# Performance work log

Hardware: AMD Instinct MI355X
Metric: run time of the kernel (lower is better)

The kernel has to match this reference:

```python
import jax, jax.numpy as jnp
import numpy as np

N_NODES = 50000
N_EDGES = 800000


def _gcn_conv(x, W, b, src, dst, n_nodes):
    # GCNConv(normalize=False): out[i] = sum_{(j->i) in E} (x_j @ W) + b
    h = x @ W                                   # [N, d_out]
    agg = jax.ops.segment_sum(h[src], dst, num_segments=n_nodes)  # [N, d_out]
    return agg + b


def setup_inputs() -> dict:
    key = jax.random.key(0)
    ks = jax.random.split(key, 10)
    nfeat, nhid, nclass = 500, 64, 50
    inp = {
        "features": jax.random.normal(ks[0], (N_NODES, nfeat), dtype=jnp.float32),
        "edge_index": jax.random.randint(ks[1], (2, N_EDGES), 0, N_NODES, dtype=jnp.int64),
        "W1": jax.random.normal(ks[2], (nfeat, nhid), dtype=jnp.float32) * (1.0 / np.sqrt(nfeat)),
        "b1": jax.random.normal(ks[3], (nhid,), dtype=jnp.float32) * 0.01,
        "Wc1": jax.random.normal(ks[4], (nhid, nhid), dtype=jnp.float32) * (1.0 / np.sqrt(nhid)),
        "bc1": jax.random.normal(ks[5], (nhid,), dtype=jnp.float32) * 0.01,
        "Wc2": jax.random.normal(ks[6], (2 * nhid, 2 * nhid), dtype=jnp.float32) * (1.0 / np.sqrt(2 * nhid)),
        "bc2": jax.random.normal(ks[7], (2 * nhid,), dtype=jnp.float32) * 0.01,
        "W2": jax.random.normal(ks[8], (7 * nhid, nclass), dtype=jnp.float32) * (1.0 / np.sqrt(7 * nhid)),
        "b2": jax.random.normal(ks[9], (nclass,), dtype=jnp.float32) * 0.01,
    }
    return inp


def reference(features, edge_index, W1, b1, Wc1, bc1, Wc2, bc2, W2, b2):
    n = features.shape[0]
    src, dst = edge_index[0], edge_index[1]  # PyG: messages flow row(src) -> col(dst)

    x = jax.nn.relu(features @ W1 + b1)                       # [N, nhid]
    x11 = _gcn_conv(x, Wc1, bc1, src, dst, n)                 # [N, nhid]
    x12 = _gcn_conv(x11, Wc1, bc1, src, dst, n)               # [N, nhid]
    x1 = jnp.concatenate((x11, x12), axis=-1)                 # [N, 2*nhid]
    x21 = _gcn_conv(x1, Wc2, bc2, src, dst, n)                # [N, 2*nhid]
    x22 = _gcn_conv(x21, Wc2, bc2, src, dst, n)               # [N, 2*nhid]
    x2 = jnp.concatenate((x21, x22), axis=-1)                 # [N, 4*nhid]
    h = jnp.concatenate((x, x1, x2), axis=-1)                 # [N, 7*nhid]
    # dropout omitted (deterministic inference reference)
    return jax.nn.sigmoid(h @ W2 + b2)                        # [N, nclass]
```

## Files before the change

### kernel.cpp

```cpp
#include <hip/hip_runtime.h>
#include <math.h>

#define N_NODES 50000
#define N_EDGES 800000

typedef short bf16x8 __attribute__((ext_vector_type(8)));
typedef float f32x4 __attribute__((ext_vector_type(4)));

__device__ __forceinline__ ushort f2bf(float f) {
    unsigned u = __float_as_uint(f);
    u += 0x7fffu + ((u >> 16) & 1u);
    return (ushort)(u >> 16);
}
__device__ __forceinline__ float bf2f(ushort h) {
    return __uint_as_float(((unsigned)h) << 16);
}
__device__ __forceinline__ void split2(float a, ushort& h, ushort& l) {
    h = f2bf(a);
    l = f2bf(a - bf2f(h));
}

__global__ __launch_bounds__(256) void convert_wt_kernel(
    const float* __restrict__ W, int K, int N, int KP, int NP,
    ushort* __restrict__ Th, ushort* __restrict__ Tl)
{
    int i = blockIdx.x * 256 + threadIdx.x;
    if (i >= NP * KP) return;
    int n = i / KP, k = i % KP;
    float v = (k < K && n < N) ? W[(size_t)k * N + n] : 0.f;
    ushort h, l;
    split2(v, h, l);
    Th[(size_t)n * KP + k] = h;
    Tl[(size_t)n * KP + k] = l;
}

__device__ __forceinline__ void stage_B_lds(
    const ushort* __restrict__ WTh, const ushort* __restrict__ WTl,
    int n0, int KP, int k0, ushort* sBh, ushort* sBl, int tid)
{
    for (int i = tid; i < 512; i += 256) {
        int pl = i >> 8, s = i & 255, row = s >> 2, q = s & 3;
        const ushort* src = pl ? WTl : WTh;
        uint4 v = *(const uint4*)&src[(size_t)(n0 + row) * KP + k0 + q * 8];
        ushort* d = pl ? sBl : sBh;
        *(uint4*)&d[row * 40 + q * 8] = v;
    }
}

__device__ __forceinline__ void stage_A_planes(
    const ushort* __restrict__ Ahi, const ushort* __restrict__ Alo,
    int lda, int brow, int M, int k0, ushort* sAh, ushort* sAl, int tid)
{
    for (int i = tid; i < 1024; i += 256) {
        int pl = i >> 9, s = i & 511, row = s >> 2, q = s & 3;
        int gr = brow + row;
        uint4 v = make_uint4(0u, 0u, 0u, 0u);
        const ushort* src = pl ? Alo : Ahi;
        if (gr < M) v = *(const uint4*)&src[(size_t)gr * lda + k0 + q * 8];
        ushort* d = pl ? sAl : sAh;
        *(uint4*)&d[row * 40 + q * 8] = v;
    }
}

__device__ __forceinline__ void mfma_compute(
    const ushort* sAh, const ushort* sAl,
    const ushort* sBh, const ushort* sBl,
    int lane, int wr, int wc, f32x4 acc[4][2])
{
    bf16x8 ah[4], al[4], bh[2], bl[2];
#pragma unroll
    for (int mi = 0; mi < 4; ++mi) {
        int off = (wr + mi * 16 + (lane & 15)) * 40 + (lane >> 4) * 8;
        ah[mi] = *(const bf16x8*)&sAh[off];
        al[mi] = *(const bf16x8*)&sAl[off];
    }
#pragma unroll
    for (int ni = 0; ni < 2; ++ni) {
        int off = (wc + ni * 16 + (lane & 15)) * 40 + (lane >> 4) * 8;
        bh[ni] = *(const bf16x8*)&sBh[off];
        bl[ni] = *(const bf16x8*)&sBl[off];
    }
#pragma unroll
    for (int mi = 0; mi < 4; ++mi)
#pragma unroll
        for (int ni = 0; ni < 2; ++ni) {
            acc[mi][ni] = __builtin_amdgcn_mfma_f32_16x16x32_bf16(ah[mi], bh[ni], acc[mi][ni], 0, 0, 0);
            acc[mi][ni] = __builtin_amdgcn_mfma_f32_16x16x32_bf16(ah[mi], bl[ni], acc[mi][ni], 0, 0, 0);
            acc[mi][ni] = __builtin_amdgcn_mfma_f32_16x16x32_bf16(al[mi], bh[ni], acc[mi][ni], 0, 0, 0);
        }
}

template<int K, int ACT>
__global__ __launch_bounds__(256) void gemm_mfma_kernel(
    const ushort* __restrict__ Ahi, const ushort* __restrict__ Alo, int lda,
    const ushort* __restrict__ WTh, const ushort* __restrict__ WTl,
    const float* __restrict__ bias,
    ushort* __restrict__ Ohi, ushort* __restrict__ Olo, int ldo, int M)
{
    __shared__ ushort sAh[128 * 40], sAl[128 * 40], sBh[64 * 40], sBl[64 * 40];
    const int tid  = threadIdx.x;
    const int brow = blockIdx.x * 128;
    const int n0   = blockIdx.y * 64;
    const int lane = tid & 63, w = tid >> 6;
    const int wr = (w >> 1) * 64, wc = (w & 1) * 32;

    f32x4 acc[4][2];
#pragma unroll
    for (int mi = 0; mi < 4; ++mi)
#pragma unroll
        for (int ni = 0; ni < 2; ++ni) acc[mi][ni] = (f32x4)0.f;

    for (int ch = 0; ch < K / 32; ++ch) {
        const int k0 = ch * 32;
        stage_A_planes(Ahi, Alo, lda, brow, M, k0, sAh, sAl, tid);
        stage_B_lds(WTh, WTl, n0, K, k0, sBh, sBl, tid);
        __syncthreads();
        mfma_compute(sAh, sAl, sBh, sBl, lane, wr, wc, acc);
        __syncthreads();
    }

#pragma unroll
    for (int mi = 0; mi < 4; ++mi)
#pragma unroll
        for (int ni = 0; ni < 2; ++ni) {
            int col = n0 + wc + ni * 16 + (lane & 15);
            float b = bias[col];
#pragma unroll
            for (int r = 0; r < 4; ++r) {
                int row = brow + wr + mi * 16 + (lane >> 4) * 4 + r;
                if (row < M) {
                    float v = acc[mi][ni][r] + b;
                    if (ACT == 1) v = fmaxf(v, 0.f);
                    ushort h, l;
                    split2(v, h, l);
                    Ohi[(size_t)row * ldo + col] = h;
                    Olo[(size_t)row * ldo + col] = l;
                }
            }
        }
}

__global__ __launch_bounds__(256) void gemm_feat_kernel(
    const float* __restrict__ A,
    const ushort* __restrict__ WTh, const ushort* __restrict__ WTl,
    const float* __restrict__ bias,
    ushort* __restrict__ Ohi, ushort* __restrict__ Olo, int M)
{
    __shared__ ushort sAh[128 * 40], sAl[128 * 40], sBh[64 * 40], sBl[64 * 40];
    const int tid  = threadIdx.x;
    const int brow = blockIdx.x * 128;
    const int lane = tid & 63, w = tid >> 6;
    const int wr = (w >> 1) * 64, wc = (w & 1) * 32;

    f32x4 acc[4][2];
#pragma unroll
    for (int mi = 0; mi < 4; ++mi)
#pragma unroll
        for (int ni = 0; ni < 2; ++ni) acc[mi][ni] = (f32x4)0.f;

    for (int ch = 0; ch < 16; ++ch) {
        const int k0 = ch * 32;
        for (int i = tid; i < 1024; i += 256) {
            int row = i >> 3, q = i & 7;
            int gr = brow + row, gk = k0 + q * 4;
            float4 v = make_float4(0.f, 0.f, 0.f, 0.f);
            if (gr < M) {
                const float* ap = A + (size_t)gr * 500;
                if (gk + 3 < 500) {
                    v = *(const float4*)&ap[gk];
                } else {
                    if (gk + 0 < 500) v.x = ap[gk + 0];
                    if (gk + 1 < 500) v.y = ap[gk + 1];
                    if (gk + 2 < 500) v.z = ap[gk + 2];
                    if (gk + 3 < 500) v.w = ap[gk + 3];
                }
            }
            ushort h0, h1, h2, h3, l0, l1, l2, l3;
            split2(v.x, h0, l0); split2(v.y, h1, l1);
            split2(v.z, h2, l2); split2(v.w, h3, l3);
            uint2 hv, lv;
            hv.x = (unsigned)h0 | ((unsigned)h1 << 16);
            hv.y = (unsigned)h2 | ((unsigned)h3 << 16);
            lv.x = (unsigned)l0 | ((unsigned)l1 << 16);
            lv.y = (unsigned)l2 | ((unsigned)l3 << 16);
            *(uint2*)&sAh[row * 40 + q * 4] = hv;
            *(uint2*)&sAl[row * 40 + q * 4] = lv;
        }
        stage_B_lds(WTh, WTl, 0, 512, k0, sBh, sBl, tid);
        __syncthreads();
        mfma_compute(sAh, sAl, sBh, sBl, lane, wr, wc, acc);
        __syncthreads();
    }

#pragma unroll
    for (int mi = 0; mi < 4; ++mi)
#pragma unroll
        for (int ni = 0; ni < 2; ++ni) {
            int col = wc + ni * 16 + (lane & 15);
            float b = bias[col];
#pragma unroll
            for (int r = 0; r < 4; ++r) {
                int row = brow + wr + mi * 16 + (lane >> 4) * 4 + r;
                if (row < M) {
                    float v = fmaxf(acc[mi][ni][r] + b, 0.f);
                    ushort h, l;
                    split2(v, h, l);
                    Ohi[(size_t)row * 64 + col] = h;
                    Olo[(size_t)row * 64 + col] = l;
                }
            }
        }
}

__global__ __launch_bounds__(256) void final_mfma_kernel(
    const ushort* __restrict__ Xhi,  const ushort* __restrict__ Xlo,
    const ushort* __restrict__ X1hi, const ushort* __restrict__ X1lo,
    const ushort* __restrict__ X2hi, const ushort* __restrict__ X2lo,
    const ushort* __restrict__ WTh,  const ushort* __restrict__ WTl,
    const float* __restrict__ b2,
    float* __restrict__ out, int M)
{
    __shared__ ushort sAh[128 * 40], sAl[128 * 40], sBh[64 * 40], sBl[64 * 40];
    const int tid  = threadIdx.x;
    const int brow = blockIdx.x * 128;
    const int lane = tid & 63, w = tid >> 6;
    const int wr = (w >> 1) * 64, wc = (w & 1) * 32;

    f32x4 acc[4][2];
#pragma unroll
    for (int mi = 0; mi < 4; ++mi)
#pragma unroll
        for (int ni = 0; ni < 2; ++ni) acc[mi][ni] = (f32x4)0.f;

    for (int ch = 0; ch < 14; ++ch) {
        const ushort *Ah, *Al;
        int lda, off;
        if (ch < 2)      { Ah = Xhi;  Al = Xlo;  lda = 64;  off = ch * 32; }
        else if (ch < 6) { Ah = X1hi; Al = X1lo; lda = 128; off = (ch - 2) * 32; }
        else             { Ah = X2hi; Al = X2lo; lda = 256; off = (ch - 6) * 32; }
        stage_A_planes(Ah + off, Al + off, lda, brow, M, 0, sAh, sAl, tid);
        stage_B_lds(WTh, WTl, 0, 448, ch * 32, sBh, sBl, tid);
        __syncthreads();
        mfma_compute(sAh, sAl, sBh, sBl, lane, wr, wc, acc);
        __syncthreads();
    }

#pragma unroll
    for (int mi = 0; mi < 4; ++mi)
#pragma unroll
        for (int ni = 0; ni < 2; ++ni) {
            int col = wc + ni * 16 + (lane & 15);
            if (col < 50) {
                float b = b2[col];
#pragma unroll
                for (int r = 0; r < 4; ++r) {
                    int row = brow + wr + mi * 16 + (lane >> 4) * 4 + r;
                    if (row < M) {
                        float v = acc[mi][ni][r] + b;
                        out[(size_t)row * 50 + col] = 1.f / (1.f + expf(-v));
                    }
                }
            }
        }
}

__global__ __launch_bounds__(256) void zero_kernel(int* __restrict__ p, int n)
{
    int i = blockIdx.x * 256 + threadIdx.x;
    if (i < n) p[i] = 0;
}

__global__ __launch_bounds__(256) void count_kernel(
    const int* __restrict__ dst, int* __restrict__ counts, int ne)
{
    int e = blockIdx.x * 256 + threadIdx.x;
    if (e < ne) atomicAdd(&counts[dst[e]], 1);
}

__global__ __launch_bounds__(256) void scan1_kernel(
    const int* __restrict__ counts, int* __restrict__ local,
    int* __restrict__ bsum, int n)
{
    __shared__ int sd[256];
    const int t = threadIdx.x;
    const int i = blockIdx.x * 256 + t;
    int c = (i < n) ? counts[i] : 0;
    sd[t] = c;
    __syncthreads();
#pragma unroll
    for (int off = 1; off < 256; off <<= 1) {
        int v = (t >= off) ? sd[t - off] : 0;
        __syncthreads();
        sd[t] += v;
        __syncthreads();
    }
    if (i < n) local[i] = sd[t] - c;
    if (t == 255) bsum[blockIdx.x] = sd[255];
}

__global__ __launch_bounds__(256) void scan2_kernel(
    const int* __restrict__ bsum, int* __restrict__ boff, int nb)
{
    __shared__ int sd[256];
    const int t = threadIdx.x;
    int v = (t < nb) ? bsum[t] : 0;
    sd[t] = v;
    __syncthreads();
#pragma unroll
    for (int off = 1; off < 256; off <<= 1) {
        int u = (t >= off) ? sd[t - off] : 0;
        __syncthreads();
        sd[t] += u;
        __syncthreads();
    }
    if (t < nb) boff[t] = sd[t] - v;
}

__global__ __launch_bounds__(256) void scan3_kernel(
    int* __restrict__ row_ptr, const int* __restrict__ boff,
    int* __restrict__ cursor, int n, int total)
{
    const int i = blockIdx.x * 256 + threadIdx.x;
    if (i < n) {
        int v = row_ptr[i] + boff[blockIdx.x];
        row_ptr[i] = v;
        cursor[i]  = v;
    }
    if (i == 0) row_ptr[n] = total;
}

__global__ __launch_bounds__(256) void fill_kernel(
    const int* __restrict__ src, const int* __restrict__ dst,
    int* __restrict__ cursor, int* __restrict__ elist, int ne)
{
    int e = blockIdx.x * 256 + threadIdx.x;
    if (e < ne) {
        int p = atomicAdd(&cursor[dst[e]], 1);
        elist[p] = src[e];
    }
}

template<int D>
__global__ __launch_bounds__(256) void agg_planes_kernel(
    const ushort* __restrict__ hhi, const ushort* __restrict__ hlo, int ldh,
    const int* __restrict__ row_ptr, const int* __restrict__ elist,
    ushort* __restrict__ ohi, ushort* __restrict__ olo, int ldo, int n)
{
    constexpr int LPR = D / 4;
    constexpr int EPI = 64 / LPR;
    const int lane = threadIdx.x & 63;
    const int node = blockIdx.x * 4 + (threadIdx.x >> 6);
    if (node >= n) return;
    const int g  = lane / LPR;
    const int c4 = (lane % LPR) * 4;
    const int beg = row_ptr[node], end = row_ptr[node + 1];

    float a0 = 0.f, a1 = 0.f, a2 = 0.f, a3 = 0.f;
    for (int e = beg + g; e < end; e += EPI) {
        int s = elist[e];
        uint2 hv = *(const uint2*)&hhi[(size_t)s * ldh + c4];
        uint2 lv = *(const uint2*)&hlo[(size_t)s * ldh + c4];
        a0 += bf2f((ushort)hv.x) + bf2f((ushort)lv.x);
        a1 += bf2f((ushort)(hv.x >> 16)) + bf2f((ushort)(lv.x >> 16));
        a2 += bf2f((ushort)hv.y) + bf2f((ushort)lv.y);
        a3 += bf2f((ushort)(hv.y >> 16)) + bf2f((ushort)(lv.y >> 16));
    }
    if (EPI == 4) {
        a0 += __shfl_xor(a0, 16); a1 += __shfl_xor(a1, 16);
        a2 += __shfl_xor(a2, 16); a3 += __shfl_xor(a3, 16);
    }
    a0 += __shfl_xor(a0, 32); a1 += __shfl_xor(a1, 32);
    a2 += __shfl_xor(a2, 32); a3 += __shfl_xor(a3, 32);

    if (g == 0) {
        ushort h0, h1, h2, h3, l0, l1, l2, l3;
        split2(a0, h0, l0); split2(a1, h1, l1);
        split2(a2, h2, l2); split2(a3, h3, l3);
        uint2 hv, lv;
        hv.x = (unsigned)h0 | ((unsigned)h1 << 16);
        hv.y = (unsigned)h2 | ((unsigned)h3 << 16);
        lv.x = (unsigned)l0 | ((unsigned)l1 << 16);
        lv.y = (unsigned)l2 | ((unsigned)l3 << 16);
        *(uint2*)&ohi[(size_t)node * ldo + c4] = hv;
        *(uint2*)&olo[(size_t)node * ldo + c4] = lv;
    }
}

extern "C" void kernel_launch(void* const* d_in, const int* in_sizes, int n_in,
                              void* d_out, int out_size, void* d_ws, size_t ws_size,
                              hipStream_t stream)
{
    const float* features = (const float*)d_in[0];
    const int*   ei       = (const int*)d_in[1];
    const float* W1  = (const float*)d_in[2];
    const float* b1  = (const float*)d_in[3];
    const float* Wc1 = (const float*)d_in[4];
    const float* bc1 = (const float*)d_in[5];
    const float* Wc2 = (const float*)d_in[6];
    const float* bc2 = (const float*)d_in[7];
    const float* W2  = (const float*)d_in[8];
    const float* b2  = (const float*)d_in[9];
    float* out = (float*)d_out;

    const int* src = ei;
    const int* dst = ei + N_EDGES;

    ushort* Xhi  = (ushort*)d_ws;
    ushort* Xlo  = Xhi  + (size_t)N_NODES * 64;
    ushort* X1hi = Xlo  + (size_t)N_NODES * 64;
    ushort* X1lo = X1hi + (size_t)N_NODES * 128;
    ushort* X2hi = X1lo + (size_t)N_NODES * 128;
    ushort* X2lo = X2hi + (size_t)N_NODES * 256;
    ushort* Ghi  = X2lo + (size_t)N_NODES * 256;
    ushort* Glo  = Ghi  + (size_t)N_NODES * 128;
    ushort* W1Th  = Glo  + (size_t)N_NODES * 128;
    ushort* W1Tl  = W1Th  + 64 * 512;
    ushort* Wc1Th = W1Tl  + 64 * 512;
    ushort* Wc1Tl = Wc1Th + 64 * 64;
    ushort* Wc2Th = Wc1Tl + 64 * 64;
    ushort* Wc2Tl = Wc2Th + 128 * 128;
    ushort* W2Th  = Wc2Tl + 128 * 128;
    ushort* W2Tl  = W2Th  + 64 * 448;
    int* counts  = (int*)(W2Tl + 64 * 448);
    int* cursor  = counts + N_NODES;
    int* row_ptr = cursor + N_NODES;
    int* elist   = row_ptr + (N_NODES + 1);
    int* bsum    = elist + N_EDGES;
    int* boff    = bsum + 256;

    const int MB = (N_NODES + 127) / 128;
    const int EB = (N_EDGES + 255) / 256;
    const int NB = (N_NODES + 255) / 256;
    const int AB = (N_NODES + 3) / 4;

    zero_kernel<<<NB, 256, 0, stream>>>(counts, N_NODES);
    count_kernel<<<EB, 256, 0, stream>>>(dst, counts, N_EDGES);
    scan1_kernel<<<NB, 256, 0, stream>>>(counts, row_ptr, bsum, N_NODES);
    scan2_kernel<<<1, 256, 0, stream>>>(bsum, boff, NB);
    scan3_kernel<<<NB, 256, 0, stream>>>(row_ptr, boff, cursor, N_NODES, N_EDGES);
    fill_kernel<<<EB, 256, 0, stream>>>(src, dst, cursor, elist, N_EDGES);

    convert_wt_kernel<<<(64 * 512 + 255) / 256, 256, 0, stream>>>(W1, 500, 64, 512, 64, W1Th, W1Tl);
    convert_wt_kernel<<<(64 * 64 + 255) / 256, 256, 0, stream>>>(Wc1, 64, 64, 64, 64, Wc1Th, Wc1Tl);
    convert_wt_kernel<<<(128 * 128 + 255) / 256, 256, 0, stream>>>(Wc2, 128, 128, 128, 128, Wc2Th, Wc2Tl);
    convert_wt_kernel<<<(64 * 448 + 255) / 256, 256, 0, stream>>>(W2, 448, 50, 448, 64, W2Th, W2Tl);

    gemm_feat_kernel<<<MB, 256, 0, stream>>>(features, W1Th, W1Tl, b1, Xhi, Xlo, N_NODES);

    agg_planes_kernel<64><<<AB, 256, 0, stream>>>(Xhi, Xlo, 64, row_ptr, elist, Ghi, Glo, 128, N_NODES);
    gemm_mfma_kernel<64, 0><<<dim3(MB, 1), 256, 0, stream>>>(
        Ghi, Glo, 128, Wc1Th, Wc1Tl, bc1, X1hi, X1lo, 128, N_NODES);

    agg_planes_kernel<64><<<AB, 256, 0, stream>>>(X1hi, X1lo, 128, row_ptr, elist, Ghi, Glo, 128, N_NODES);
    gemm_mfma_kernel<64, 0><<<dim3(MB, 1), 256, 0, stream>>>(
        Ghi, Glo, 128, Wc1Th, Wc1Tl, bc1, X1hi + 64, X1lo + 64, 128, N_NODES);

    agg_planes_kernel<64><<<AB, 256, 0, stream>>>(X1hi + 64, X1lo + 64, 128, row_ptr, elist,
                                                  Ghi + 64, Glo + 64, 128, N_NODES);
    gemm_mfma_kernel<128, 0><<<dim3(MB, 2), 256, 0, stream>>>(
        Ghi, Glo, 128, Wc2Th, Wc2Tl, bc2, X2hi, X2lo, 256, N_NODES);

    agg_planes_kernel<128><<<AB, 256, 0, stream>>>(X2hi, X2lo, 256, row_ptr, elist, Ghi, Glo, 128, N_NODES);
    gemm_mfma_kernel<128, 0><<<dim3(MB, 2), 256, 0, stream>>>(
        Ghi, Glo, 128, Wc2Th, Wc2Tl, bc2, X2hi + 128, X2lo + 128, 256, N_NODES);

    final_mfma_kernel<<<MB, 256, 0, stream>>>(Xhi, Xlo, X1hi, X1lo, X2hi, X2lo,
                                              W2Th, W2Tl, b2, out, N_NODES);
}
```

Baseline: 576.0 us.

## Register-prefetch GEMM tiles, shrink row tile to 64, unroll edge aggregation by two

The GEMM kernels now prefetch the next K-chunk of A and B into registers while the MFMAs run on the current LDS tile. This hides global load latency behind compute. The row tile also drops from 128 to 64, which doubles the block count for better occupancy and SM fill but reuses B less per block. The aggregation loop is unrolled by two so more gather loads are in flight per lane.

```diff
diff --git a/kernel.cpp b/kernel.cpp
--- a/kernel.cpp
+++ b/kernel.cpp
@@ -34,42 +34,56 @@
     Tl[(size_t)n * KP + k] = l;
 }
 
-__device__ __forceinline__ void stage_B_lds(
+__device__ __forceinline__ void loadA_planes(
+    const ushort* __restrict__ Ahi, const ushort* __restrict__ Alo,
+    int lda, int brow, int M, int k0, int tid, uint4* pA)
+{
+#pragma unroll
+    for (int j = 0; j < 2; ++j) {
+        int i = j * 256 + tid;
+        int pl = i >> 8, s = i & 255, row = s >> 2, q = s & 3;
+        int gr = brow + row;
+        const ushort* src = pl ? Alo : Ahi;
+        uint4 v = make_uint4(0u, 0u, 0u, 0u);
+        if (gr < M) v = *(const uint4*)&src[(size_t)gr * lda + k0 + q * 8];
+        pA[j] = v;
+    }
+}
+
+__device__ __forceinline__ void loadB_planes(
     const ushort* __restrict__ WTh, const ushort* __restrict__ WTl,
-    int n0, int KP, int k0, ushort* sBh, ushort* sBl, int tid)
-{
-    for (int i = tid; i < 512; i += 256) {
+    int n0, int KP, int k0, int tid, uint4* pB)
+{
+#pragma unroll
+    for (int j = 0; j < 2; ++j) {
+        int i = j * 256 + tid;
         int pl = i >> 8, s = i & 255, row = s >> 2, q = s & 3;
         const ushort* src = pl ? WTl : WTh;
-        uint4 v = *(const uint4*)&src[(size_t)(n0 + row) * KP + k0 + q * 8];
-        ushort* d = pl ? sBl : sBh;
-        *(uint4*)&d[row * 40 + q * 8] = v;
-    }
-}
-
-__device__ __forceinline__ void stage_A_planes(
-    const ushort* __restrict__ Ahi, const ushort* __restrict__ Alo,
-    int lda, int brow, int M, int k0, ushort* sAh, ushort* sAl, int tid)
-{
-    for (int i = tid; i < 1024; i += 256) {
-        int pl = i >> 9, s = i & 511, row = s >> 2, q = s & 3;
-        int gr = brow + row;
-        uint4 v = make_uint4(0u, 0u, 0u, 0u);
-        const ushort* src = pl ? Alo : Ahi;
-        if (gr < M) v = *(const uint4*)&src[(size_t)gr * lda + k0 + q * 8];
-        ushort* d = pl ? sAl : sAh;
-        *(uint4*)&d[row * 40 + q * 8] = v;
-    }
-}
-
-__device__ __forceinline__ void mfma_compute(
+        pB[j] = *(const uint4*)&src[(size_t)(n0 + row) * KP + k0 + q * 8];
+    }
+}
+
+__device__ __forceinline__ void writeAB(
+    ushort* sAh, ushort* sAl, ushort* sBh, ushort* sBl,
+    int tid, const uint4* pA, const uint4* pB)
+{
+#pragma unroll
+    for (int j = 0; j < 2; ++j) {
+        int i = j * 256 + tid;
+        int pl = i >> 8, s = i & 255, row = s >> 2, q = s & 3;
+        *(uint4*)&(pl ? sAl : sAh)[row * 40 + q * 8] = pA[j];
+        *(uint4*)&(pl ? sBl : sBh)[row * 40 + q * 8] = pB[j];
+    }
+}
+
+__device__ __forceinline__ void mfma_2x2(
     const ushort* sAh, const ushort* sAl,
     const ushort* sBh, const ushort* sBl,
-    int lane, int wr, int wc, f32x4 acc[4][2])
-{
-    bf16x8 ah[4], al[4], bh[2], bl[2];
-#pragma unroll
-    for (int mi = 0; mi < 4; ++mi) {
+    int lane, int wr, int wc, f32x4 acc[2][2])
+{
+    bf16x8 ah[2], al[2], bh[2], bl[2];
+#pragma unroll
+    for (int mi = 0; mi < 2; ++mi) {
         int off = (wr + mi * 16 + (lane & 15)) * 40 + (lane >> 4) * 8;
         ah[mi] = *(const bf16x8*)&sAh[off];
         al[mi] = *(const bf16x8*)&sAl[off];
@@ -81,7 +95,7 @@
         bl[ni] = *(const bf16x8*)&sBl[off];
     }
 #pragma unroll
-    for (int mi = 0; mi < 4; ++mi)
+    for (int mi = 0; mi < 2; ++mi)
 #pragma unroll
         for (int ni = 0; ni < 2; ++ni) {
             acc[mi][ni] = __builtin_amdgcn_mfma_f32_16x16x32_bf16(ah[mi], bh[ni], acc[mi][ni], 0, 0, 0);
@@ -97,30 +111,37 @@
     const float* __restrict__ bias,
     ushort* __restrict__ Ohi, ushort* __restrict__ Olo, int ldo, int M)
 {
-    __shared__ ushort sAh[128 * 40], sAl[128 * 40], sBh[64 * 40], sBl[64 * 40];
+    constexpr int NCH = K / 32;
+    __shared__ ushort sAh[64 * 40], sAl[64 * 40], sBh[64 * 40], sBl[64 * 40];
     const int tid  = threadIdx.x;
-    const int brow = blockIdx.x * 128;
+    const int brow = blockIdx.x * 64;
     const int n0   = blockIdx.y * 64;
     const int lane = tid & 63, w = tid >> 6;
-    const int wr = (w >> 1) * 64, wc = (w & 1) * 32;
-
-    f32x4 acc[4][2];
-#pragma unroll
-    for (int mi = 0; mi < 4; ++mi)
+    const int wr = (w >> 1) * 32, wc = (w & 1) * 32;
+
+    f32x4 acc[2][2];
+#pragma unroll
+    for (int mi = 0; mi < 2; ++mi)
 #pragma unroll
         for (int ni = 0; ni < 2; ++ni) acc[mi][ni] = (f32x4)0.f;
 
-    for (int ch = 0; ch < K / 32; ++ch) {
-        const int k0 = ch * 32;
-        stage_A_planes(Ahi, Alo, lda, brow, M, k0, sAh, sAl, tid);
-        stage_B_lds(WTh, WTl, n0, K, k0, sBh, sBl, tid);
-        __syncthreads();
-        mfma_compute(sAh, sAl, sBh, sBl, lane, wr, wc, acc);
-        __syncthreads();
-    }
-
-#pragma unroll
-    for (int mi = 0; mi < 4; ++mi)
+    uint4 pA[2], pB[2];
+    loadA_planes(Ahi, Alo, lda, brow, M, 0, tid, pA);
+    loadB_planes(WTh, WTl, n0, K, 0, tid, pB);
+
+    for (int ch = 0; ch < NCH; ++ch) {
+        writeAB(sAh, sAl, sBh, sBl, tid, pA, pB);
+        __syncthreads();
+        if (ch + 1 < NCH) {
+            loadA_planes(Ahi, Alo, lda, brow, M, (ch + 1) * 32, tid, pA);
+            loadB_planes(WTh, WTl, n0, K, (ch + 1) * 32, tid, pB);
+        }
+        mfma_2x2(sAh, sAl, sBh, sBl, lane, wr, wc, acc);
+        __syncthreads();
+    }
+
+#pragma unroll
+    for (int mi = 0; mi < 2; ++mi)
 #pragma unroll
         for (int ni = 0; ni < 2; ++ni) {
             int col = n0 + wc + ni * 16 + (lane & 15);
@@ -146,22 +167,26 @@
     const float* __restrict__ bias,
     ushort* __restrict__ Ohi, ushort* __restrict__ Olo, int M)
 {
-    __shared__ ushort sAh[128 * 40], sAl[128 * 40], sBh[64 * 40], sBl[64 * 40];
+    __shared__ ushort sAh[64 * 40], sAl[64 * 40], sBh[64 * 40], sBl[64 * 40];
     const int tid  = threadIdx.x;
-    const int brow = blockIdx.x * 128;
+    const int brow = blockIdx.x * 64;
     const int lane = tid & 63, w = tid >> 6;
-    const int wr = (w >> 1) * 64, wc = (w & 1) * 32;
-
-    f32x4 acc[4][2];
-#pragma unroll
-    for (int mi = 0; mi < 4; ++mi)
+    const int wr = (w >> 1) * 32, wc = (w & 1) * 32;
+
+    f32x4 acc[2][2];
+#pragma unroll
+    for (int mi = 0; mi < 2; ++mi)
 #pragma unroll
         for (int ni = 0; ni < 2; ++ni) acc[mi][ni] = (f32x4)0.f;
 
-    for (int ch = 0; ch < 16; ++ch) {
-        const int k0 = ch * 32;
-        for (int i = tid; i < 1024; i += 256) {
-            int row = i >> 3, q = i & 7;
+    const int frow = tid >> 2, fq = (tid & 3);
+    float4 pA[2];
+    uint4  pB[2];
+
+    auto loadA_feat = [&](int k0) {
+#pragma unroll
+        for (int j = 0; j < 2; ++j) {
+            int row = frow, q = fq + j * 4;
             int gr = brow + row, gk = k0 + q * 4;
             float4 v = make_float4(0.f, 0.f, 0.f, 0.f);
             if (gr < M) {
@@ -175,9 +200,16 @@
                     if (gk + 3 < 500) v.w = ap[gk + 3];
                 }
             }
+            pA[j] = v;
+        }
+    };
+    auto writeA_feat = [&]() {
+#pragma unroll
+        for (int j = 0; j < 2; ++j) {
+            int row = frow, q = fq + j * 4;
             ushort h0, h1, h2, h3, l0, l1, l2, l3;
-            split2(v.x, h0, l0); split2(v.y, h1, l1);
-            split2(v.z, h2, l2); split2(v.w, h3, l3);
+            split2(pA[j].x, h0, l0); split2(pA[j].y, h1, l1);
+            split2(pA[j].z, h2, l2); split2(pA[j].w, h3, l3);
             uint2 hv, lv;
             hv.x = (unsigned)h0 | ((unsigned)h1 << 16);
             hv.y = (unsigned)h2 | ((unsigned)h3 << 16);
@@ -186,14 +218,30 @@
             *(uint2*)&sAh[row * 40 + q * 4] = hv;
             *(uint2*)&sAl[row * 40 + q * 4] = lv;
         }
-        stage_B_lds(WTh, WTl, 0, 512, k0, sBh, sBl, tid);
-        __syncthreads();
-        mfma_compute(sAh, sAl, sBh, sBl, lane, wr, wc, acc);
-        __syncthreads();
-    }
-
-#pragma unroll
-    for (int mi = 0; mi < 4; ++mi)
+    };
+
+    loadA_feat(0);
+    loadB_planes(WTh, WTl, 0, 512, 0, tid, pB);
+
+    for (int ch = 0; ch < 16; ++ch) {
+        writeA_feat();
+#pragma unroll
+        for (int j = 0; j < 2; ++j) {
+            int i = j * 256 + tid;
+            int pl = i >> 8, s = i & 255, row = s >> 2, q = s & 3;
+            *(uint4*)&(pl ? sBl : sBh)[row * 40 + q * 8] = pB[j];
+        }
+        __syncthreads();
+        if (ch + 1 < 16) {
+            loadA_feat((ch + 1) * 32);
+            loadB_planes(WTh, WTl, 0, 512, (ch + 1) * 32, tid, pB);
+        }
+        mfma_2x2(sAh, sAl, sBh, sBl, lane, wr, wc, acc);
+        __syncthreads();
+    }
+
+#pragma unroll
+    for (int mi = 0; mi < 2; ++mi)
 #pragma unroll
         for (int ni = 0; ni < 2; ++ni) {
             int col = wc + ni * 16 + (lane & 15);
@@ -220,33 +268,47 @@
     const float* __restrict__ b2,
     float* __restrict__ out, int M)
 {
-    __shared__ ushort sAh[128 * 40], sAl[128 * 40], sBh[64 * 40], sBl[64 * 40];
+    __shared__ ushort sAh[64 * 40], sAl[64 * 40], sBh[64 * 40], sBl[64 * 40];
     const int tid  = threadIdx.x;
-    const int brow = blockIdx.x * 128;
+    const int brow = blockIdx.x * 64;
     const int lane = tid & 63, w = tid >> 6;
-    const int wr = (w >> 1) * 64, wc = (w & 1) * 32;
-
-    f32x4 acc[4][2];
-#pragma unroll
-    for (int mi = 0; mi < 4; ++mi)
+    const int wr = (w >> 1) * 32, wc = (w & 1) * 32;
+
+    f32x4 acc[2][2];
+#pragma unroll
+    for (int mi = 0; mi < 2; ++mi)
 #pragma unroll
         for (int ni = 0; ni < 2; ++ni) acc[mi][ni] = (f32x4)0.f;
 
+    auto getsrc = [&](int ch, const ushort*& Ah, const ushort*& Al, int& lda) {
+        if (ch < 2)      { Ah = Xhi  + ch * 32;       Al = Xlo  + ch * 32;       lda = 64;  }
+        else if (ch < 6) { Ah = X1hi + (ch - 2) * 32; Al = X1lo + (ch - 2) * 32; lda = 128; }
+        else             { Ah = X2hi + (ch - 6) * 32; Al = X2lo + (ch - 6) * 32; lda = 256; }
+    };
+
+    uint4 pA[2], pB[2];
+    {
+        const ushort *Ah, *Al; int lda;
+        getsrc(0, Ah, Al, lda);
+        loadA_planes(Ah, Al, lda, brow, M, 0, tid, pA);
+    }
+    loadB_planes(WTh, WTl, 0, 448, 0, tid, pB);
+
     for (int ch = 0; ch < 14; ++ch) {
-        const ushort *Ah, *Al;
-        int lda, off;
-        if (ch < 2)      { Ah = Xhi;  Al = Xlo;  lda = 64;  off = ch * 32; }
-        else if (ch < 6) { Ah = X1hi; Al = X1lo; lda = 128; off = (ch - 2) * 32; }
-        else             { Ah = X2hi; Al = X2lo; lda = 256; off = (ch - 6) * 32; }
-        stage_A_planes(Ah + off, Al + off, lda, brow, M, 0, sAh, sAl, tid);
-        stage_B_lds(WTh, WTl, 0, 448, ch * 32, sBh, sBl, tid);
-        __syncthreads();
-        mfma_compute(sAh, sAl, sBh, sBl, lane, wr, wc, acc);
-        __syncthreads();
-    }
-
-#pragma unroll
-    for (int mi = 0; mi < 4; ++mi)
+        writeAB(sAh, sAl, sBh, sBl, tid, pA, pB);
+        __syncthreads();
+        if (ch + 1 < 14) {
+            const ushort *Ah, *Al; int lda;
+            getsrc(ch + 1, Ah, Al, lda);
+            loadA_planes(Ah, Al, lda, brow, M, 0, tid, pA);
+            loadB_planes(WTh, WTl, 0, 448, (ch + 1) * 32, tid, pB);
+        }
+        mfma_2x2(sAh, sAl, sBh, sBl, lane, wr, wc, acc);
+        __syncthreads();
+    }
+
+#pragma unroll
+    for (int mi = 0; mi < 2; ++mi)
 #pragma unroll
         for (int ni = 0; ni < 2; ++ni) {
             int col = wc + ni * 16 + (lane & 15);
@@ -356,14 +418,30 @@
     const int beg = row_ptr[node], end = row_ptr[node + 1];
 
     float a0 = 0.f, a1 = 0.f, a2 = 0.f, a3 = 0.f;
-    for (int e = beg + g; e < end; e += EPI) {
-        int s = elist[e];
-        uint2 hv = *(const uint2*)&hhi[(size_t)s * ldh + c4];
-        uint2 lv = *(const uint2*)&hlo[(size_t)s * ldh + c4];
-        a0 += bf2f((ushort)hv.x) + bf2f((ushort)lv.x);
-        a1 += bf2f((ushort)(hv.x >> 16)) + bf2f((ushort)(lv.x >> 16));
-        a2 += bf2f((ushort)hv.y) + bf2f((ushort)lv.y);
-        a3 += bf2f((ushort)(hv.y >> 16)) + bf2f((ushort)(lv.y >> 16));
+    int e = beg + g;
+    for (; e + EPI < end; e += 2 * EPI) {
+        int s0 = elist[e], s1 = elist[e + EPI];
+        uint2 h0 = *(const uint2*)&hhi[(size_t)s0 * ldh + c4];
+        uint2 l0 = *(const uint2*)&hlo[(size_t)s0 * ldh + c4];
+        uint2 h1 = *(const uint2*)&hhi[(size_t)s1 * ldh + c4];
+        uint2 l1 = *(const uint2*)&hlo[(size_t)s1 * ldh + c4];
+        a0 += bf2f((ushort)h0.x) + bf2f((ushort)l0.x)
+            + bf2f((ushort)h1.x) + bf2f((ushort)l1.x);
+        a1 += bf2f((ushort)(h0.x >> 16)) + bf2f((ushort)(l0.x >> 16))
+            + bf2f((ushort)(h1.x >> 16)) + bf2f((ushort)(l1.x >> 16));
+        a2 += bf2f((ushort)h0.y) + bf2f((ushort)l0.y)
+            + bf2f((ushort)h1.y) + bf2f((ushort)l1.y);
+        a3 += bf2f((ushort)(h0.y >> 16)) + bf2f((ushort)(l0.y >> 16))
+            + bf2f((ushort)(h1.y >> 16)) + bf2f((ushort)(l1.y >> 16));
+    }
+    if (e < end) {
+        int s0 = elist[e];
+        uint2 h0 = *(const uint2*)&hhi[(size_t)s0 * ldh + c4];
+        uint2 l0 = *(const uint2*)&hlo[(size_t)s0 * ldh + c4];
+        a0 += bf2f((ushort)h0.x) + bf2f((ushort)l0.x);
+        a1 += bf2f((ushort)(h0.x >> 16)) + bf2f((ushort)(l0.x >> 16));
+        a2 += bf2f((ushort)h0.y) + bf2f((ushort)l0.y);
+        a3 += bf2f((ushort)(h0.y >> 16)) + bf2f((ushort)(l0.y >> 16));
     }
     if (EPI == 4) {
         a0 += __shfl_xor(a0, 16); a1 += __shfl_xor(a1, 16);
@@ -428,7 +506,7 @@
     int* bsum    = elist + N_EDGES;
     int* boff    = bsum + 256;
 
-    const int MB = (N_NODES + 127) / 128;
+    const int MB = (N_NODES + 63) / 64;
     const int EB = (N_EDGES + 255) / 256;
     const int NB = (N_NODES + 255) / 256;
     const int AB = (N_NODES + 3) / 4;
```

New measurement: 589.1 us. 2.3% more time.
